# Kernel tuning notes

Measured on AMD Instinct MI355X. Metric: run time of the kernel, lower is better.

## Reference

```python
import jax, jax.numpy as jnp
import numpy as np

N_NODES = 100000
N_EDGES = 1600000
IN_DIM = 64
HIDDEN = 128
CLASSES = 3
N_MATERIALS = 8


def setup_inputs() -> dict:
    key = jax.random.key(0)
    ks = jax.random.split(key, 12)
    def lin(k, fan_in, fan_out):
        bound = 1.0 / np.sqrt(fan_in)
        kw, kb = jax.random.split(k)
        W = jax.random.uniform(kw, (fan_in, fan_out), jnp.float32, -bound, bound)
        b = jax.random.uniform(kb, (fan_out,), jnp.float32, -bound, bound)
        return W, b
    x = jax.random.normal(ks[0], (N_NODES, IN_DIM), jnp.float32)
    edge_index = jax.random.randint(ks[1], (2, N_EDGES), 0, N_NODES, jnp.int64)
    Wl1, b1 = lin(ks[2], IN_DIM, HIDDEN)   # SAGEConv lin_l (agg, with bias)
    Wr1, _ = lin(ks[3], IN_DIM, HIDDEN)    # SAGEConv lin_r (root, no bias)
    Wl2, b2 = lin(ks[4], HIDDEN, HIDDEN)
    Wr2, _ = lin(ks[5], HIDDEN, HIDDEN)
    Wh, bh = lin(ks[6], HIDDEN, CLASSES)
    Wm, bm = lin(ks[7], HIDDEN, N_MATERIALS)
    return {"x": x, "edge_index": edge_index,
            "Wl1": Wl1, "Wr1": Wr1, "b1": b1,
            "Wl2": Wl2, "Wr2": Wr2, "b2": b2,
            "Wh": Wh, "bh": bh, "Wm": Wm, "bm": bm}


def _sage_conv(x, src, dst, Wl, Wr, b, n_nodes):
    # mean-aggregate source features at destination nodes, then linear + root linear
    msg = x[src]                                               # [E, F]
    agg = jax.ops.segment_sum(msg, dst, num_segments=n_nodes)  # [N, F]
    deg = jax.ops.segment_sum(jnp.ones((src.shape[0],), x.dtype), dst,
                              num_segments=n_nodes)            # [N]
    agg = agg / jnp.maximum(deg, 1.0)[:, None]
    return agg @ Wl + x @ Wr + b


def reference(x, edge_index, Wl1, Wr1, b1, Wl2, Wr2, b2, Wh, bh, Wm, bm):
    src, dst = edge_index[0], edge_index[1]
    n = x.shape[0]
    h = jax.nn.relu(_sage_conv(x, src, dst, Wl1, Wr1, b1, n))
    # dropout(p=0.35) is identity in eval mode
    h = jax.nn.relu(_sage_conv(h, src, dst, Wl2, Wr2, b2, n))
    return (h @ Wh + bh, h @ Wm + bm)
```

## Files before the change

kernel.cpp:

```cpp
#include <hip/hip_runtime.h>

#define N_NODES 100000
#define N_EDGES 1600000
#define NBUCK 196
#define BSH 9

typedef __attribute__((ext_vector_type(8))) short short8;
typedef __attribute__((ext_vector_type(4))) float f32x4;

__device__ __forceinline__ float bflo(unsigned int u) { return __uint_as_float(u << 16); }
__device__ __forceinline__ float bfhi(unsigned int u) { return __uint_as_float(u & 0xffff0000u); }
__device__ __forceinline__ float bf2f(unsigned short u) { return __uint_as_float(((unsigned int)u) << 16); }
__device__ __forceinline__ unsigned short f2bf(float f) {
    unsigned int u = __float_as_uint(f);
    return (unsigned short)((u + 0x7fffu + ((u >> 16) & 1u)) >> 16);
}

__global__ __launch_bounds__(256) void k_cast_hist(const float* __restrict__ x, unsigned short* __restrict__ xh,
                                                   const int* __restrict__ dst, int* __restrict__ deg) {
    int i = blockIdx.x * 256 + threadIdx.x;
    float4 v = *reinterpret_cast<const float4*>(x + (size_t)i * 4);
    ushort4 o;
    o.x = f2bf(v.x); o.y = f2bf(v.y); o.z = f2bf(v.z); o.w = f2bf(v.w);
    *reinterpret_cast<ushort4*>(xh + (size_t)i * 4) = o;
    atomicAdd(&deg[dst[i]], 1);
}

__global__ __launch_bounds__(1024) void k_part_scan(const int* __restrict__ deg,
                                                    int* __restrict__ rowstart, int* __restrict__ bsum) {
    __shared__ int wsum[16];
    const int tid = threadIdx.x, lane = tid & 63, wid = tid >> 6;
    int i = blockIdx.x * 1024 + tid;
    int v = (i < N_NODES) ? deg[i] : 0;
    int s = v;
    #pragma unroll
    for (int off = 1; off < 64; off <<= 1) {
        int t = __shfl_up(s, off);
        if (lane >= off) s += t;
    }
    if (lane == 63) wsum[wid] = s;
    __syncthreads();
    if (tid < 16) {
        int w = wsum[tid];
        #pragma unroll
        for (int off = 1; off < 16; off <<= 1) {
            int t = __shfl_up(w, off);
            if (tid >= off) w += t;
        }
        wsum[tid] = w;
    }
    __syncthreads();
    int wexcl = (wid == 0) ? 0 : wsum[wid - 1];
    if (i < N_NODES) rowstart[i] = wexcl + s - v;
    if (tid == 1023) bsum[blockIdx.x] = wexcl + s;
}

__global__ __launch_bounds__(128) void k_scan_bsum(const int* __restrict__ bsum, int* __restrict__ boff,
                                                   int* __restrict__ rowstart, int nblk) {
    __shared__ int sh[128];
    int t = threadIdx.x;
    int v = (t < nblk) ? bsum[t] : 0;
    int acc = v;
    sh[t] = acc;
    __syncthreads();
    #pragma unroll
    for (int off = 1; off < 128; off <<= 1) {
        int add = (t >= off) ? sh[t - off] : 0;
        __syncthreads();
        acc += add;
        sh[t] = acc;
        __syncthreads();
    }
    if (t < nblk) boff[t] = acc - v;
    if (t == nblk - 1) rowstart[N_NODES] = acc;
}

__global__ __launch_bounds__(1024) void k_add_off(const int* __restrict__ boff, int* __restrict__ rowstart) {
    int i = blockIdx.x * 1024 + threadIdx.x;
    if (i < N_NODES) rowstart[i] += boff[blockIdx.x];
}

__global__ __launch_bounds__(256) void k_init_ccur(const int* __restrict__ rowstart, int* __restrict__ ccur) {
    int t = threadIdx.x;
    if (t < NBUCK) ccur[t] = rowstart[t << BSH];
}

#define EPT 16
__global__ __launch_bounds__(256) void k_bucket(const int* __restrict__ src, const int* __restrict__ dst,
                                                int* __restrict__ ccur, unsigned int* __restrict__ pairs) {
    __shared__ int cnt[NBUCK];
    __shared__ int base[NBUCK];
    const int tid = threadIdx.x;
    const int e_base = blockIdx.x * (256 * EPT);
    for (int i = tid; i < NBUCK; i += 256) cnt[i] = 0;
    __syncthreads();
    #pragma unroll
    for (int i = 0; i < EPT; ++i) {
        int e = e_base + i * 256 + tid;
        if (e < N_EDGES) atomicAdd(&cnt[dst[e] >> BSH], 1);
    }
    __syncthreads();
    for (int i = tid; i < NBUCK; i += 256) {
        int c = cnt[i];
        base[i] = (c > 0) ? atomicAdd(&ccur[i], c) : 0;
        cnt[i] = 0;
    }
    __syncthreads();
    #pragma unroll
    for (int i = 0; i < EPT; ++i) {
        int e = e_base + i * 256 + tid;
        if (e < N_EDGES) {
            int d = dst[e];
            int bkt = d >> BSH;
            int off = atomicAdd(&cnt[bkt], 1);
            pairs[base[bkt] + off] = ((unsigned int)(d & 511) << 17) | (unsigned int)src[e];
        }
    }
}

__global__ __launch_bounds__(256) void k_scatter_csr(const int* __restrict__ rowstart,
                                                     const unsigned int* __restrict__ pairs,
                                                     int* __restrict__ srcs) {
    __shared__ int lcur[512];
    const int c = blockIdx.x, tid = threadIdx.x;
    const int nbase = c << BSH;
    for (int i = tid; i < 512; i += 256) {
        int n = nbase + i;
        lcur[i] = (n < N_NODES) ? rowstart[n] : 0;
    }
    __syncthreads();
    int e0 = rowstart[nbase];
    int nend = nbase + 512; if (nend > N_NODES) nend = N_NODES;
    int e1 = rowstart[nend];
    for (int e = e0 + tid; e < e1; e += 256) {
        unsigned int u = pairs[e];
        int dloc = (int)(u >> 17);
        int p = atomicAdd(&lcur[dloc], 1);
        srcs[p] = (int)(u & 0x1FFFFu);
    }
}

__global__ __launch_bounds__(256) void k_pack(const float* __restrict__ Wl1, const float* __restrict__ Wr1,
                                              const float* __restrict__ Wl2, const float* __restrict__ Wr2,
                                              unsigned short* __restrict__ Bp1, unsigned short* __restrict__ Bp2) {
    int idx = blockIdx.x * 256 + threadIdx.x;
    if (idx < 16384) {
        int j = idx & 7, g = (idx >> 3) & 3, col = (idx >> 5) & 127, kk = idx >> 12;
        int r = kk * 32 + g * 8 + j;
        float w = (r < 64) ? Wl1[r * 128 + col] : Wr1[(r - 64) * 128 + col];
        Bp1[idx] = f2bf(w);
    } else {
        int q = idx - 16384;
        int j = q & 7, g = (q >> 3) & 3, col = (q >> 5) & 127, kk = q >> 12;
        int r = kk * 32 + g * 8 + j;
        float w = (r < 128) ? Wl2[r * 128 + col] : Wr2[(r - 128) * 128 + col];
        Bp2[q] = f2bf(w);
    }
}

__global__ __launch_bounds__(256, 8) void k_layer1(
    const unsigned short* __restrict__ xh,
    const int* __restrict__ rowstart, const int* __restrict__ srcs,
    const unsigned short* __restrict__ Bp1, const float* __restrict__ b,
    unsigned short* __restrict__ h1h)
{
    __shared__ unsigned short A[32][136];
    __shared__ int rs[33];
    const int tile = blockIdx.x * 32;
    const int tid = threadIdx.x, lane = tid & 63, wid = tid >> 6;

    if (tid < 33) rs[tid] = rowstart[tile + tid];
    {
        int node = tid >> 3, part = tid & 7;
        uint4 v = *reinterpret_cast<const uint4*>(xh + (size_t)(tile + node) * 64 + part * 8);
        *reinterpret_cast<uint4*>(&A[node][64 + part * 8]) = v;
    }
    __syncthreads();

    for (int it = 0; it < 8; ++it) {
        int nl = wid * 8 + it;
        int e0 = rs[nl], e1 = rs[nl + 1];
        float a0 = 0.f, a1 = 0.f, a2 = 0.f, a3 = 0.f;
        int e = e0;
        for (; e + 8 <= e1; e += 8) {
            int s0 = srcs[e],     s1 = srcs[e + 1], s2 = srcs[e + 2], s3 = srcs[e + 3];
            int s4 = srcs[e + 4], s5 = srcs[e + 5], s6 = srcs[e + 6], s7 = srcs[e + 7];
            float v0 = bf2f(xh[(size_t)s0 * 64 + lane]);
            float v1 = bf2f(xh[(size_t)s1 * 64 + lane]);
            float v2 = bf2f(xh[(size_t)s2 * 64 + lane]);
            float v3 = bf2f(xh[(size_t)s3 * 64 + lane]);
            float v4 = bf2f(xh[(size_t)s4 * 64 + lane]);
            float v5 = bf2f(xh[(size_t)s5 * 64 + lane]);
            float v6 = bf2f(xh[(size_t)s6 * 64 + lane]);
            float v7 = bf2f(xh[(size_t)s7 * 64 + lane]);
            a0 += v0; a1 += v1; a2 += v2; a3 += v3;
            a0 += v4; a1 += v5; a2 += v6; a3 += v7;
        }
        for (; e < e1; ++e)
            a0 += bf2f(xh[(size_t)srcs[e] * 64 + lane]);
        float acc = (a0 + a1) + (a2 + a3);
        int d = e1 - e0;
        A[nl][lane] = f2bf(acc * ((d > 0) ? (1.0f / (float)d) : 1.0f));
    }
    __syncthreads();

    const int r15 = lane & 15, g4 = lane >> 4;
    const int n0 = wid * 32;
    f32x4 acc[2][2] = {};
    for (int kk = 0; kk < 4; ++kk) {
        short8 b0 = *reinterpret_cast<const short8*>(Bp1 + (((kk * 128 + n0 + r15) * 4 + g4) << 3));
        short8 b1 = *reinterpret_cast<const short8*>(Bp1 + (((kk * 128 + n0 + 16 + r15) * 4 + g4) << 3));
        #pragma unroll
        for (int mt = 0; mt < 2; ++mt) {
            short8 a = *reinterpret_cast<const short8*>(&A[mt * 16 + r15][kk * 32 + g4 * 8]);
            acc[mt][0] = __builtin_amdgcn_mfma_f32_16x16x32_bf16(a, b0, acc[mt][0], 0, 0, 0);
            acc[mt][1] = __builtin_amdgcn_mfma_f32_16x16x32_bf16(a, b1, acc[mt][1], 0, 0, 0);
        }
    }
    #pragma unroll
    for (int mt = 0; mt < 2; ++mt)
        #pragma unroll
        for (int nt = 0; nt < 2; ++nt) {
            int col = n0 + nt * 16 + r15;
            float bb = b[col];
            #pragma unroll
            for (int reg = 0; reg < 4; ++reg) {
                int row = tile + mt * 16 + g4 * 4 + reg;
                h1h[(size_t)row * 128 + col] = f2bf(fmaxf(acc[mt][nt][reg] + bb, 0.0f));
            }
        }
}

__global__ __launch_bounds__(256, 8) void k_layer2(
    const unsigned int* __restrict__ h1h32,
    const int* __restrict__ rowstart, const int* __restrict__ srcs,
    const unsigned short* __restrict__ Bp2, const float* __restrict__ b,
    const float* __restrict__ Wh, const float* __restrict__ bh,
    const float* __restrict__ Wm, const float* __restrict__ bm,
    float* __restrict__ out1, float* __restrict__ out2)
{
    __shared__ unsigned short A[32][264];
    __shared__ int rs[33];
    const int tile = blockIdx.x * 32;
    const int tid = threadIdx.x, lane = tid & 63, wid = tid >> 6;

    if (tid < 33) rs[tid] = rowstart[tile + tid];
    {
        int node = tid >> 3, part = tid & 7;
        const unsigned int* p = h1h32 + (size_t)(tile + node) * 64 + part * 8;
        uint4 v0 = *reinterpret_cast<const uint4*>(p);
        uint4 v1 = *reinterpret_cast<const uint4*>(p + 4);
        *reinterpret_cast<uint4*>(&A[node][128 + part * 16]) = v0;
        *reinterpret_cast<uint4*>(&A[node][128 + part * 16 + 8]) = v1;
    }
    __syncthreads();

    for (int it = 0; it < 8; ++it) {
        int nl = wid * 8 + it;
        int e0 = rs[nl], e1 = rs[nl + 1];
        float ax0 = 0.f, ax1 = 0.f, ax2 = 0.f, ax3 = 0.f;
        float ay0 = 0.f, ay1 = 0.f, ay2 = 0.f, ay3 = 0.f;
        int e = e0;
        for (; e + 8 <= e1; e += 8) {
            int s0 = srcs[e],     s1 = srcs[e + 1], s2 = srcs[e + 2], s3 = srcs[e + 3];
            int s4 = srcs[e + 4], s5 = srcs[e + 5], s6 = srcs[e + 6], s7 = srcs[e + 7];
            unsigned int u0 = h1h32[(size_t)s0 * 64 + lane];
            unsigned int u1 = h1h32[(size_t)s1 * 64 + lane];
            unsigned int u2 = h1h32[(size_t)s2 * 64 + lane];
            unsigned int u3 = h1h32[(size_t)s3 * 64 + lane];
            unsigned int u4 = h1h32[(size_t)s4 * 64 + lane];
            unsigned int u5 = h1h32[(size_t)s5 * 64 + lane];
            unsigned int u6 = h1h32[(size_t)s6 * 64 + lane];
            unsigned int u7 = h1h32[(size_t)s7 * 64 + lane];
            ax0 += bflo(u0); ay0 += bfhi(u0);
            ax1 += bflo(u1); ay1 += bfhi(u1);
            ax2 += bflo(u2); ay2 += bfhi(u2);
            ax3 += bflo(u3); ay3 += bfhi(u3);
            ax0 += bflo(u4); ay0 += bfhi(u4);
            ax1 += bflo(u5); ay1 += bfhi(u5);
            ax2 += bflo(u6); ay2 += bfhi(u6);
            ax3 += bflo(u7); ay3 += bfhi(u7);
        }
        for (; e < e1; ++e) {
            unsigned int u = h1h32[(size_t)srcs[e] * 64 + lane];
            ax0 += bflo(u); ay0 += bfhi(u);
        }
        float ax = (ax0 + ax1) + (ax2 + ax3);
        float ay = (ay0 + ay1) + (ay2 + ay3);
        int d = e1 - e0;
        float rd = (d > 0) ? (1.0f / (float)d) : 1.0f;
        unsigned int p = (unsigned int)f2bf(ax * rd) | ((unsigned int)f2bf(ay * rd) << 16);
        *reinterpret_cast<unsigned int*>(&A[nl][2 * lane]) = p;
    }
    __syncthreads();

    const int r15 = lane & 15, g4 = lane >> 4;
    const int n0 = wid * 32;
    f32x4 acc[2][2] = {};
    for (int kk = 0; kk < 8; ++kk) {
        short8 b0 = *reinterpret_cast<const short8*>(Bp2 + (((kk * 128 + n0 + r15) * 4 + g4) << 3));
        short8 b1 = *reinterpret_cast<const short8*>(Bp2 + (((kk * 128 + n0 + 16 + r15) * 4 + g4) << 3));
        #pragma unroll
        for (int mt = 0; mt < 2; ++mt) {
            short8 a = *reinterpret_cast<const short8*>(&A[mt * 16 + r15][kk * 32 + g4 * 8]);
            acc[mt][0] = __builtin_amdgcn_mfma_f32_16x16x32_bf16(a, b0, acc[mt][0], 0, 0, 0);
            acc[mt][1] = __builtin_amdgcn_mfma_f32_16x16x32_bf16(a, b1, acc[mt][1], 0, 0, 0);
        }
    }
    __syncthreads();
    float* h2L = reinterpret_cast<float*>(&A[0][0]);
    #pragma unroll
    for (int mt = 0; mt < 2; ++mt)
        #pragma unroll
        for (int nt = 0; nt < 2; ++nt) {
            int col = n0 + nt * 16 + r15;
            float bb = b[col];
            #pragma unroll
            for (int reg = 0; reg < 4; ++reg) {
                int row = mt * 16 + g4 * 4 + reg;
                h2L[row * 132 + col] = fmaxf(acc[mt][nt][reg] + bb, 0.0f);
            }
        }
    __syncthreads();

    for (int t = tid; t < 352; t += 256) {
        int node = t / 11, o = t - node * 11;
        const float* h2 = &h2L[node * 132];
        if (o < 3) {
            float s = bh[o];
            for (int k = 0; k < 128; ++k) s += h2[k] * Wh[k * 3 + o];
            out1[(size_t)(tile + node) * 3 + o] = s;
        } else {
            int m = o - 3;
            float s = bm[m];
            for (int k = 0; k < 128; ++k) s += h2[k] * Wm[k * 8 + m];
            out2[(size_t)(tile + node) * 8 + m] = s;
        }
    }
}

extern "C" void kernel_launch(void* const* d_in, const int* in_sizes, int n_in,
                              void* d_out, int out_size, void* d_ws, size_t ws_size,
                              hipStream_t stream) {
    const float* x   = (const float*)d_in[0];
    const int*   ei  = (const int*)d_in[1];
    const int*   src = ei;
    const int*   dst = ei + N_EDGES;
    const float* Wl1 = (const float*)d_in[2];
    const float* Wr1 = (const float*)d_in[3];
    const float* b1  = (const float*)d_in[4];
    const float* Wl2 = (const float*)d_in[5];
    const float* Wr2 = (const float*)d_in[6];
    const float* b2  = (const float*)d_in[7];
    const float* Wh  = (const float*)d_in[8];
    const float* bh  = (const float*)d_in[9];
    const float* Wm  = (const float*)d_in[10];
    const float* bm  = (const float*)d_in[11];

    float* out1 = (float*)d_out;
    float* out2 = out1 + (size_t)N_NODES * 3;

    char* ws = (char*)d_ws;
    int*   deg      = (int*)(ws);
    int*   rowstart = (int*)(ws + (512 << 10));
    int*   bsum     = (int*)(ws + (960 << 10));
    int*   boff     = (int*)(ws + (1024 << 10));
    int*   ccur     = (int*)(ws + (1088 << 10));
    unsigned int* pairs = (unsigned int*)(ws + (1536 << 10));
    int*   srcs     = (int*)(ws + (8192 << 10));
    unsigned short* xh  = (unsigned short*)(ws + (15360 << 10));
    unsigned short* h1h = (unsigned short*)(ws + (28672 << 10));
    unsigned short* Bp1 = (unsigned short*)(ws + (54784 << 10));
    unsigned short* Bp2 = (unsigned short*)(ws + (54848 << 10));

    const int NSCAN = (N_NODES + 1023) / 1024;
    const int NBKT_BLKS = (N_EDGES + 256 * EPT - 1) / (256 * EPT);

    hipMemsetAsync(deg, 0, N_NODES * sizeof(int), stream);
    k_cast_hist<<<6250, 256, 0, stream>>>(x, xh, dst, deg);
    k_part_scan<<<NSCAN, 1024, 0, stream>>>(deg, rowstart, bsum);
    k_scan_bsum<<<1, 128, 0, stream>>>(bsum, boff, rowstart, NSCAN);
    k_add_off<<<NSCAN, 1024, 0, stream>>>(boff, rowstart);
    k_init_ccur<<<1, 256, 0, stream>>>(rowstart, ccur);
    k_bucket<<<NBKT_BLKS, 256, 0, stream>>>(src, dst, ccur, pairs);
    k_scatter_csr<<<NBUCK, 256, 0, stream>>>(rowstart, pairs, srcs);
    k_pack<<<192, 256, 0, stream>>>(Wl1, Wr1, Wl2, Wr2, Bp1, Bp2);

    k_layer1<<<3125, 256, 0, stream>>>(xh, rowstart, srcs, Bp1, b1, h1h);
    k_layer2<<<3125, 256, 0, stream>>>((const unsigned int*)h1h, rowstart, srcs,
                                       Bp2, b2, Wh, bh, Wm, bm, out1, out2);
}
```

Before: 318.0 us.

## Vectorize neighbor gathers with 16-byte loads across edges and fold ccur init

The aggregation loops in both layers now gather whole 16-byte chunks of a neighbor row per lane, with lane groups handling different edges at once. Partial sums are then combined with xor shuffles and written as packed bf16 vectors. This replaces scalar 2- and 4-byte per-lane loads with fewer, wider memory transactions. The bucket cursor initialization is folded into the block-offset scan kernel, which drops one launch; it computes the bucket start from the partially scanned rowstart plus the block's exclusive offset. The cost is extra shuffle reductions per node and idle lanes in the tail loop.

```diff
diff --git a/kernel.cpp b/kernel.cpp
--- a/kernel.cpp
+++ b/kernel.cpp
@@ -10,10 +10,12 @@
 
 __device__ __forceinline__ float bflo(unsigned int u) { return __uint_as_float(u << 16); }
 __device__ __forceinline__ float bfhi(unsigned int u) { return __uint_as_float(u & 0xffff0000u); }
-__device__ __forceinline__ float bf2f(unsigned short u) { return __uint_as_float(((unsigned int)u) << 16); }
 __device__ __forceinline__ unsigned short f2bf(float f) {
     unsigned int u = __float_as_uint(f);
     return (unsigned short)((u + 0x7fffu + ((u >> 16) & 1u)) >> 16);
+}
+__device__ __forceinline__ unsigned int pk2(float a, float b) {
+    return (unsigned int)f2bf(a) | ((unsigned int)f2bf(b) << 16);
 }
 
 __global__ __launch_bounds__(256) void k_cast_hist(const float* __restrict__ x, unsigned short* __restrict__ xh,
@@ -56,8 +58,9 @@
 }
 
 __global__ __launch_bounds__(128) void k_scan_bsum(const int* __restrict__ bsum, int* __restrict__ boff,
-                                                   int* __restrict__ rowstart, int nblk) {
+                                                   int* __restrict__ rowstart, int* __restrict__ ccur, int nblk) {
     __shared__ int sh[128];
+    __shared__ int excl[128];
     int t = threadIdx.x;
     int v = (t < nblk) ? bsum[t] : 0;
     int acc = v;
@@ -72,17 +75,16 @@
         __syncthreads();
     }
     if (t < nblk) boff[t] = acc - v;
+    excl[t] = acc - v;
     if (t == nblk - 1) rowstart[N_NODES] = acc;
+    __syncthreads();
+    for (int c = t; c < NBUCK; c += 128)
+        ccur[c] = rowstart[c << BSH] + excl[c >> 1];
 }
 
 __global__ __launch_bounds__(1024) void k_add_off(const int* __restrict__ boff, int* __restrict__ rowstart) {
     int i = blockIdx.x * 1024 + threadIdx.x;
     if (i < N_NODES) rowstart[i] += boff[blockIdx.x];
-}
-
-__global__ __launch_bounds__(256) void k_init_ccur(const int* __restrict__ rowstart, int* __restrict__ ccur) {
-    int t = threadIdx.x;
-    if (t < NBUCK) ccur[t] = rowstart[t << BSH];
 }
 
 #define EPT 16
@@ -172,35 +174,53 @@
     if (tid < 33) rs[tid] = rowstart[tile + tid];
     {
         int node = tid >> 3, part = tid & 7;
-        uint4 v = *reinterpret_cast<const uint4*>(xh + (size_t)(tile + node) * 64 + part * 8);
+        uint4 v = *reinterpret_cast<const uint4*>(xh + (((unsigned)(tile + node)) << 6) + part * 8);
         *reinterpret_cast<uint4*>(&A[node][64 + part * 8]) = v;
     }
     __syncthreads();
 
+    const int g = lane >> 3;
+    const int q = lane & 7;
     for (int it = 0; it < 8; ++it) {
         int nl = wid * 8 + it;
         int e0 = rs[nl], e1 = rs[nl + 1];
-        float a0 = 0.f, a1 = 0.f, a2 = 0.f, a3 = 0.f;
+        float f0 = 0.f, f1 = 0.f, f2 = 0.f, f3 = 0.f, f4 = 0.f, f5 = 0.f, f6 = 0.f, f7 = 0.f;
         int e = e0;
         for (; e + 8 <= e1; e += 8) {
-            int s0 = srcs[e],     s1 = srcs[e + 1], s2 = srcs[e + 2], s3 = srcs[e + 3];
-            int s4 = srcs[e + 4], s5 = srcs[e + 5], s6 = srcs[e + 6], s7 = srcs[e + 7];
-            float v0 = bf2f(xh[(size_t)s0 * 64 + lane]);
-            float v1 = bf2f(xh[(size_t)s1 * 64 + lane]);
-            float v2 = bf2f(xh[(size_t)s2 * 64 + lane]);
-            float v3 = bf2f(xh[(size_t)s3 * 64 + lane]);
-            float v4 = bf2f(xh[(size_t)s4 * 64 + lane]);
-            float v5 = bf2f(xh[(size_t)s5 * 64 + lane]);
-            float v6 = bf2f(xh[(size_t)s6 * 64 + lane]);
-            float v7 = bf2f(xh[(size_t)s7 * 64 + lane]);
-            a0 += v0; a1 += v1; a2 += v2; a3 += v3;
-            a0 += v4; a1 += v5; a2 += v6; a3 += v7;
-        }
-        for (; e < e1; ++e)
-            a0 += bf2f(xh[(size_t)srcs[e] * 64 + lane]);
-        float acc = (a0 + a1) + (a2 + a3);
+            int s = srcs[e + g];
+            uint4 u = *reinterpret_cast<const uint4*>(xh + (((unsigned)s) << 6) + q * 8);
+            f0 += bflo(u.x); f1 += bfhi(u.x);
+            f2 += bflo(u.y); f3 += bfhi(u.y);
+            f4 += bflo(u.z); f5 += bfhi(u.z);
+            f6 += bflo(u.w); f7 += bfhi(u.w);
+        }
+        for (; e < e1; ++e) {
+            if (g == 0) {
+                uint4 u = *reinterpret_cast<const uint4*>(xh + (((unsigned)srcs[e]) << 6) + q * 8);
+                f0 += bflo(u.x); f1 += bfhi(u.x);
+                f2 += bflo(u.y); f3 += bfhi(u.y);
+                f4 += bflo(u.z); f5 += bfhi(u.z);
+                f6 += bflo(u.w); f7 += bfhi(u.w);
+            }
+        }
+        f0 += __shfl_xor(f0, 8); f0 += __shfl_xor(f0, 16); f0 += __shfl_xor(f0, 32);
+        f1 += __shfl_xor(f1, 8); f1 += __shfl_xor(f1, 16); f1 += __shfl_xor(f1, 32);
+        f2 += __shfl_xor(f2, 8); f2 += __shfl_xor(f2, 16); f2 += __shfl_xor(f2, 32);
+        f3 += __shfl_xor(f3, 8); f3 += __shfl_xor(f3, 16); f3 += __shfl_xor(f3, 32);
+        f4 += __shfl_xor(f4, 8); f4 += __shfl_xor(f4, 16); f4 += __shfl_xor(f4, 32);
+        f5 += __shfl_xor(f5, 8); f5 += __shfl_xor(f5, 16); f5 += __shfl_xor(f5, 32);
+        f6 += __shfl_xor(f6, 8); f6 += __shfl_xor(f6, 16); f6 += __shfl_xor(f6, 32);
+        f7 += __shfl_xor(f7, 8); f7 += __shfl_xor(f7, 16); f7 += __shfl_xor(f7, 32);
         int d = e1 - e0;
-        A[nl][lane] = f2bf(acc * ((d > 0) ? (1.0f / (float)d) : 1.0f));
+        float rd = (d > 0) ? (1.0f / (float)d) : 1.0f;
+        if (g == 0) {
+            uint4 p;
+            p.x = pk2(f0 * rd, f1 * rd);
+            p.y = pk2(f2 * rd, f3 * rd);
+            p.z = pk2(f4 * rd, f5 * rd);
+            p.w = pk2(f6 * rd, f7 * rd);
+            *reinterpret_cast<uint4*>(&A[nl][q * 8]) = p;
+        }
     }
     __syncthreads();
 
@@ -247,7 +267,7 @@
     if (tid < 33) rs[tid] = rowstart[tile + tid];
     {
         int node = tid >> 3, part = tid & 7;
-        const unsigned int* p = h1h32 + (size_t)(tile + node) * 64 + part * 8;
+        const unsigned int* p = h1h32 + (((unsigned)(tile + node)) << 6) + part * 8;
         uint4 v0 = *reinterpret_cast<const uint4*>(p);
         uint4 v1 = *reinterpret_cast<const uint4*>(p + 4);
         *reinterpret_cast<uint4*>(&A[node][128 + part * 16]) = v0;
@@ -255,42 +275,48 @@
     }
     __syncthreads();
 
+    const int g = lane >> 4;
+    const int q = lane & 15;
     for (int it = 0; it < 8; ++it) {
         int nl = wid * 8 + it;
         int e0 = rs[nl], e1 = rs[nl + 1];
-        float ax0 = 0.f, ax1 = 0.f, ax2 = 0.f, ax3 = 0.f;
-        float ay0 = 0.f, ay1 = 0.f, ay2 = 0.f, ay3 = 0.f;
+        float f0 = 0.f, f1 = 0.f, f2 = 0.f, f3 = 0.f, f4 = 0.f, f5 = 0.f, f6 = 0.f, f7 = 0.f;
         int e = e0;
-        for (; e + 8 <= e1; e += 8) {
-            int s0 = srcs[e],     s1 = srcs[e + 1], s2 = srcs[e + 2], s3 = srcs[e + 3];
-            int s4 = srcs[e + 4], s5 = srcs[e + 5], s6 = srcs[e + 6], s7 = srcs[e + 7];
-            unsigned int u0 = h1h32[(size_t)s0 * 64 + lane];
-            unsigned int u1 = h1h32[(size_t)s1 * 64 + lane];
-            unsigned int u2 = h1h32[(size_t)s2 * 64 + lane];
-            unsigned int u3 = h1h32[(size_t)s3 * 64 + lane];
-            unsigned int u4 = h1h32[(size_t)s4 * 64 + lane];
-            unsigned int u5 = h1h32[(size_t)s5 * 64 + lane];
-            unsigned int u6 = h1h32[(size_t)s6 * 64 + lane];
-            unsigned int u7 = h1h32[(size_t)s7 * 64 + lane];
-            ax0 += bflo(u0); ay0 += bfhi(u0);
-            ax1 += bflo(u1); ay1 += bfhi(u1);
-            ax2 += bflo(u2); ay2 += bfhi(u2);
-            ax3 += bflo(u3); ay3 += bfhi(u3);
-            ax0 += bflo(u4); ay0 += bfhi(u4);
-            ax1 += bflo(u5); ay1 += bfhi(u5);
-            ax2 += bflo(u6); ay2 += bfhi(u6);
-            ax3 += bflo(u7); ay3 += bfhi(u7);
+        for (; e + 4 <= e1; e += 4) {
+            int s = srcs[e + g];
+            uint4 u = *reinterpret_cast<const uint4*>(h1h32 + (((unsigned)s) << 6) + q * 4);
+            f0 += bflo(u.x); f1 += bfhi(u.x);
+            f2 += bflo(u.y); f3 += bfhi(u.y);
+            f4 += bflo(u.z); f5 += bfhi(u.z);
+            f6 += bflo(u.w); f7 += bfhi(u.w);
         }
         for (; e < e1; ++e) {
-            unsigned int u = h1h32[(size_t)srcs[e] * 64 + lane];
-            ax0 += bflo(u); ay0 += bfhi(u);
-        }
-        float ax = (ax0 + ax1) + (ax2 + ax3);
-        float ay = (ay0 + ay1) + (ay2 + ay3);
+            if (g == 0) {
+                uint4 u = *reinterpret_cast<const uint4*>(h1h32 + (((unsigned)srcs[e]) << 6) + q * 4);
+                f0 += bflo(u.x); f1 += bfhi(u.x);
+                f2 += bflo(u.y); f3 += bfhi(u.y);
+                f4 += bflo(u.z); f5 += bfhi(u.z);
+                f6 += bflo(u.w); f7 += bfhi(u.w);
+            }
+        }
+        f0 += __shfl_xor(f0, 16); f0 += __shfl_xor(f0, 32);
+        f1 += __shfl_xor(f1, 16); f1 += __shfl_xor(f1, 32);
+        f2 += __shfl_xor(f2, 16); f2 += __shfl_xor(f2, 32);
+        f3 += __shfl_xor(f3, 16); f3 += __shfl_xor(f3, 32);
+        f4 += __shfl_xor(f4, 16); f4 += __shfl_xor(f4, 32);
+        f5 += __shfl_xor(f5, 16); f5 += __shfl_xor(f5, 32);
+        f6 += __shfl_xor(f6, 16); f6 += __shfl_xor(f6, 32);
+        f7 += __shfl_xor(f7, 16); f7 += __shfl_xor(f7, 32);
         int d = e1 - e0;
         float rd = (d > 0) ? (1.0f / (float)d) : 1.0f;
-        unsigned int p = (unsigned int)f2bf(ax * rd) | ((unsigned int)f2bf(ay * rd) << 16);
-        *reinterpret_cast<unsigned int*>(&A[nl][2 * lane]) = p;
+        if (g == 0) {
+            uint4 p;
+            p.x = pk2(f0 * rd, f1 * rd);
+            p.y = pk2(f2 * rd, f3 * rd);
+            p.z = pk2(f4 * rd, f5 * rd);
+            p.w = pk2(f6 * rd, f7 * rd);
+            *reinterpret_cast<uint4*>(&A[nl][q * 8]) = p;
+        }
     }
     __syncthreads();
 
@@ -379,9 +405,8 @@
     hipMemsetAsync(deg, 0, N_NODES * sizeof(int), stream);
     k_cast_hist<<<6250, 256, 0, stream>>>(x, xh, dst, deg);
     k_part_scan<<<NSCAN, 1024, 0, stream>>>(deg, rowstart, bsum);
-    k_scan_bsum<<<1, 128, 0, stream>>>(bsum, boff, rowstart, NSCAN);
+    k_scan_bsum<<<1, 128, 0, stream>>>(bsum, boff, rowstart, ccur, NSCAN);
     k_add_off<<<NSCAN, 1024, 0, stream>>>(boff, rowstart);
-    k_init_ccur<<<1, 256, 0, stream>>>(rowstart, ccur);
     k_bucket<<<NBKT_BLKS, 256, 0, stream>>>(src, dst, ccur, pairs);
     k_scatter_csr<<<NBUCK, 256, 0, stream>>>(rowstart, pairs, srcs);
     k_pack<<<192, 256, 0, stream>>>(Wl1, Wr1, Wl2, Wr2, Bp1, Bp2);
```

Result: slower. 328.1 us (+3.2%).

## Fuse weight packing and ccur init into preprocessing kernels, refine bucket granularity

Applied to the files above, without the earlier changes.

Moves the weight-packing work into extra blocks of the cast/histogram kernel, and computes the bucket cursors inside the block-sum scan kernel, removing two kernel launches. It also halves the bucket width (256 nodes per bucket, 391 buckets) and doubles edges per thread in the bucketing pass, giving more scatter blocks and smaller shared cursor arrays. The cost is more per-block bucket counters and more global atomics on the bucket cursors. The ccur computation now depends on the excl[c>>2] mapping between 256-node buckets and 1024-node scan blocks, which has to stay consistent with the scan layout.

```diff
diff --git a/kernel.cpp b/kernel.cpp
--- a/kernel.cpp
+++ b/kernel.cpp
@@ -2,8 +2,9 @@
 
 #define N_NODES 100000
 #define N_EDGES 1600000
-#define NBUCK 196
-#define BSH 9
+#define NBUCK 391
+#define BSH 8
+#define EPT 32
 
 typedef __attribute__((ext_vector_type(8))) short short8;
 typedef __attribute__((ext_vector_type(4))) float f32x4;
@@ -16,14 +17,35 @@
     return (unsigned short)((u + 0x7fffu + ((u >> 16) & 1u)) >> 16);
 }
 
-__global__ __launch_bounds__(256) void k_cast_hist(const float* __restrict__ x, unsigned short* __restrict__ xh,
-                                                   const int* __restrict__ dst, int* __restrict__ deg) {
-    int i = blockIdx.x * 256 + threadIdx.x;
-    float4 v = *reinterpret_cast<const float4*>(x + (size_t)i * 4);
-    ushort4 o;
-    o.x = f2bf(v.x); o.y = f2bf(v.y); o.z = f2bf(v.z); o.w = f2bf(v.w);
-    *reinterpret_cast<ushort4*>(xh + (size_t)i * 4) = o;
-    atomicAdd(&deg[dst[i]], 1);
+__global__ __launch_bounds__(256) void k_cast_hist_pack(
+    const float* __restrict__ x, unsigned short* __restrict__ xh,
+    const int* __restrict__ dst, int* __restrict__ deg,
+    const float* __restrict__ Wl1, const float* __restrict__ Wr1,
+    const float* __restrict__ Wl2, const float* __restrict__ Wr2,
+    unsigned short* __restrict__ Bp1, unsigned short* __restrict__ Bp2)
+{
+    if (blockIdx.x < 6250) {
+        int i = blockIdx.x * 256 + threadIdx.x;
+        float4 v = *reinterpret_cast<const float4*>(x + (size_t)i * 4);
+        ushort4 o;
+        o.x = f2bf(v.x); o.y = f2bf(v.y); o.z = f2bf(v.z); o.w = f2bf(v.w);
+        *reinterpret_cast<ushort4*>(xh + (size_t)i * 4) = o;
+        atomicAdd(&deg[dst[i]], 1);
+    } else {
+        int idx = (blockIdx.x - 6250) * 256 + threadIdx.x;
+        if (idx < 16384) {
+            int j = idx & 7, g = (idx >> 3) & 3, col = (idx >> 5) & 127, kk = idx >> 12;
+            int r = kk * 32 + g * 8 + j;
+            float w = (r < 64) ? Wl1[r * 128 + col] : Wr1[(r - 64) * 128 + col];
+            Bp1[idx] = f2bf(w);
+        } else {
+            int q = idx - 16384;
+            int j = q & 7, g = (q >> 3) & 3, col = (q >> 5) & 127, kk = q >> 12;
+            int r = kk * 32 + g * 8 + j;
+            float w = (r < 128) ? Wl2[r * 128 + col] : Wr2[(r - 128) * 128 + col];
+            Bp2[q] = f2bf(w);
+        }
+    }
 }
 
 __global__ __launch_bounds__(1024) void k_part_scan(const int* __restrict__ deg,
@@ -56,8 +78,9 @@
 }
 
 __global__ __launch_bounds__(128) void k_scan_bsum(const int* __restrict__ bsum, int* __restrict__ boff,
-                                                   int* __restrict__ rowstart, int nblk) {
+                                                   int* __restrict__ rowstart, int* __restrict__ ccur, int nblk) {
     __shared__ int sh[128];
+    __shared__ int excl[128];
     int t = threadIdx.x;
     int v = (t < nblk) ? bsum[t] : 0;
     int acc = v;
@@ -72,7 +95,11 @@
         __syncthreads();
     }
     if (t < nblk) boff[t] = acc - v;
+    excl[t] = acc - v;
     if (t == nblk - 1) rowstart[N_NODES] = acc;
+    __syncthreads();
+    for (int c = t; c < NBUCK; c += 128)
+        ccur[c] = rowstart[c << BSH] + excl[c >> 2];
 }
 
 __global__ __launch_bounds__(1024) void k_add_off(const int* __restrict__ boff, int* __restrict__ rowstart) {
@@ -80,12 +107,6 @@
     if (i < N_NODES) rowstart[i] += boff[blockIdx.x];
 }
 
-__global__ __launch_bounds__(256) void k_init_ccur(const int* __restrict__ rowstart, int* __restrict__ ccur) {
-    int t = threadIdx.x;
-    if (t < NBUCK) ccur[t] = rowstart[t << BSH];
-}
-
-#define EPT 16
 __global__ __launch_bounds__(256) void k_bucket(const int* __restrict__ src, const int* __restrict__ dst,
                                                 int* __restrict__ ccur, unsigned int* __restrict__ pairs) {
     __shared__ int cnt[NBUCK];
@@ -113,7 +134,7 @@
             int d = dst[e];
             int bkt = d >> BSH;
             int off = atomicAdd(&cnt[bkt], 1);
-            pairs[base[bkt] + off] = ((unsigned int)(d & 511) << 17) | (unsigned int)src[e];
+            pairs[base[bkt] + off] = ((unsigned int)(d & 255) << 17) | (unsigned int)src[e];
         }
     }
 }
@@ -121,40 +142,22 @@
 __global__ __launch_bounds__(256) void k_scatter_csr(const int* __restrict__ rowstart,
                                                      const unsigned int* __restrict__ pairs,
                                                      int* __restrict__ srcs) {
-    __shared__ int lcur[512];
+    __shared__ int lcur[256];
     const int c = blockIdx.x, tid = threadIdx.x;
     const int nbase = c << BSH;
-    for (int i = tid; i < 512; i += 256) {
-        int n = nbase + i;
-        lcur[i] = (n < N_NODES) ? rowstart[n] : 0;
+    {
+        int n = nbase + tid;
+        lcur[tid] = (n < N_NODES) ? rowstart[n] : 0;
     }
     __syncthreads();
     int e0 = rowstart[nbase];
-    int nend = nbase + 512; if (nend > N_NODES) nend = N_NODES;
+    int nend = nbase + 256; if (nend > N_NODES) nend = N_NODES;
     int e1 = rowstart[nend];
     for (int e = e0 + tid; e < e1; e += 256) {
         unsigned int u = pairs[e];
         int dloc = (int)(u >> 17);
         int p = atomicAdd(&lcur[dloc], 1);
         srcs[p] = (int)(u & 0x1FFFFu);
-    }
-}
-
-__global__ __launch_bounds__(256) void k_pack(const float* __restrict__ Wl1, const float* __restrict__ Wr1,
-                                              const float* __restrict__ Wl2, const float* __restrict__ Wr2,
-                                              unsigned short* __restrict__ Bp1, unsigned short* __restrict__ Bp2) {
-    int idx = blockIdx.x * 256 + threadIdx.x;
-    if (idx < 16384) {
-        int j = idx & 7, g = (idx >> 3) & 3, col = (idx >> 5) & 127, kk = idx >> 12;
-        int r = kk * 32 + g * 8 + j;
-        float w = (r < 64) ? Wl1[r * 128 + col] : Wr1[(r - 64) * 128 + col];
-        Bp1[idx] = f2bf(w);
-    } else {
-        int q = idx - 16384;
-        int j = q & 7, g = (q >> 3) & 3, col = (q >> 5) & 127, kk = q >> 12;
-        int r = kk * 32 + g * 8 + j;
-        float w = (r < 128) ? Wl2[r * 128 + col] : Wr2[(r - 128) * 128 + col];
-        Bp2[q] = f2bf(w);
     }
 }
 
@@ -377,14 +380,12 @@
     const int NBKT_BLKS = (N_EDGES + 256 * EPT - 1) / (256 * EPT);
 
     hipMemsetAsync(deg, 0, N_NODES * sizeof(int), stream);
-    k_cast_hist<<<6250, 256, 0, stream>>>(x, xh, dst, deg);
+    k_cast_hist_pack<<<6442, 256, 0, stream>>>(x, xh, dst, deg, Wl1, Wr1, Wl2, Wr2, Bp1, Bp2);
     k_part_scan<<<NSCAN, 1024, 0, stream>>>(deg, rowstart, bsum);
-    k_scan_bsum<<<1, 128, 0, stream>>>(bsum, boff, rowstart, NSCAN);
+    k_scan_bsum<<<1, 128, 0, stream>>>(bsum, boff, rowstart, ccur, NSCAN);
     k_add_off<<<NSCAN, 1024, 0, stream>>>(boff, rowstart);
-    k_init_ccur<<<1, 256, 0, stream>>>(rowstart, ccur);
     k_bucket<<<NBKT_BLKS, 256, 0, stream>>>(src, dst, ccur, pairs);
     k_scatter_csr<<<NBUCK, 256, 0, stream>>>(rowstart, pairs, srcs);
-    k_pack<<<192, 256, 0, stream>>>(Wl1, Wr1, Wl2, Wr2, Bp1, Bp2);
 
     k_layer1<<<3125, 256, 0, stream>>>(xh, rowstart, srcs, Bp1, b1, h1h);
     k_layer2<<<3125, 256, 0, stream>>>((const unsigned int*)h1h, rowstart, srcs,
```

Result: no change. 317.5 us (-0.2%).
